# Kernel tuning notes

Measured on AMD Instinct MI355X. Metric: run time of the kernel, lower is better.

The kernel has to match this reference:

```python
import math
import jax, jax.numpy as jnp
import numpy as np

T = 4096
D_MODEL = 1024
NUM_HEADS = 16
HEAD_DIM = D_MODEL // NUM_HEADS


def setup_inputs() -> dict:
    key = jax.random.key(0)
    k_x, k_wqkv, k_wproj = jax.random.split(key, 3)
    # match eqx.nn.Linear init scale: U(-1/sqrt(in), 1/sqrt(in)); randn*small works too,
    # but keep magnitudes reasonable so softmax isn't saturated.
    s_in = 1.0 / math.sqrt(D_MODEL)
    x = jax.random.normal(k_x, (T, D_MODEL), dtype=jnp.float32)
    W_qkv = jax.random.normal(k_wqkv, (3 * D_MODEL, D_MODEL), dtype=jnp.float32) * s_in
    b_qkv = jnp.zeros((3 * D_MODEL,), dtype=jnp.float32)
    W_proj = jax.random.normal(k_wproj, (D_MODEL, D_MODEL), dtype=jnp.float32) * s_in
    b_proj = jnp.zeros((D_MODEL,), dtype=jnp.float32)
    return {"x": x, "W_qkv": W_qkv, "b_qkv": b_qkv, "W_proj": W_proj, "b_proj": b_proj}


def reference(x, W_qkv, b_qkv, W_proj, b_proj):
    T_, C = x.shape  # (seq, d_model)
    H, hd = NUM_HEADS, HEAD_DIM
    # c_attn: eqx Linear computes W @ x + b per token -> x @ W.T + b
    qkv = x @ W_qkv.T + b_qkv  # (T, 3C)
    q, k, v = jnp.split(qkv, 3, axis=1)
    # (T, C) -> (H, T, hd)
    q = q.reshape(T_, H, hd).swapaxes(0, 1)
    k = k.reshape(T_, H, hd).swapaxes(0, 1)
    v = v.reshape(T_, H, hd).swapaxes(0, 1)
    scores = jnp.einsum("htd,hsd->hts", q, k) / math.sqrt(hd)  # (H, T, T)
    causal = jnp.tril(jnp.ones((T_, T_), dtype=bool))
    scores = jnp.where(causal, scores, -jnp.inf)
    attn = jax.nn.softmax(scores, axis=-1)
    y = jnp.einsum("hts,hsd->htd", attn, v)  # (H, T, hd)
    y = y.swapaxes(0, 1).reshape(T_, C)
    y = y @ W_proj.T + b_proj
    return y
```

## Files before the change

kernel.cpp:

```cpp
#include <hip/hip_runtime.h>
#include <math.h>
#include <string.h>

#define T_SEQ 4096
#define DM 1024
#define NH 16
#define HD 64

typedef short s8v __attribute__((ext_vector_type(8)));
typedef float f4v __attribute__((ext_vector_type(4)));

__device__ inline unsigned short f2bf(float f) {
    unsigned u; memcpy(&u, &f, 4);
    u = u + 0x7fffu + ((u >> 16) & 1u);
    return (unsigned short)(u >> 16);
}

__device__ inline float bf2f(unsigned short s) {
    unsigned u = (unsigned)s << 16;
    float f; memcpy(&f, &u, 4);
    return f;
}

__device__ inline float exp2fn(float x) {
#if __has_builtin(__builtin_amdgcn_exp2f)
    return __builtin_amdgcn_exp2f(x);
#else
    return exp2f(x);
#endif
}

__device__ inline void gld_lds16(const void* g, void* l) {
    __builtin_amdgcn_global_load_lds(
        (const __attribute__((address_space(1))) void*)g,
        (__attribute__((address_space(3))) void*)l, 16, 0, 0);
}

__global__ __launch_bounds__(256)
void cvt3(const float* __restrict__ i0, unsigned short* __restrict__ o0, int n0,
          const float* __restrict__ i1, unsigned short* __restrict__ o1, int n1,
          const float* __restrict__ i2, unsigned short* __restrict__ o2, int n2) {
    int i = blockIdx.x * 256 + threadIdx.x;
    const float* in; unsigned short* out; int j;
    if (i < n0)           { in = i0; out = o0; j = i; }
    else if (i < n0 + n1) { in = i1; out = o1; j = i - n0; }
    else if (i < n0 + n1 + n2) { in = i2; out = o2; j = i - n0 - n1; }
    else return;
    const float4* p = (const float4*)(in + (size_t)j * 8);
    float4 a = p[0], b = p[1];
    unsigned short o[8] = {f2bf(a.x), f2bf(a.y), f2bf(a.z), f2bf(a.w),
                           f2bf(b.x), f2bf(b.y), f2bf(b.z), f2bf(b.w)};
    uint4 pk; memcpy(&pk, o, 16);
    *(uint4*)(out + (size_t)j * 8) = pk;
}

template<int MODE, int TN>
__global__ __launch_bounds__(256)
void gemm_bt_mfma(const unsigned short* __restrict__ A, const unsigned short* __restrict__ B,
                  const float* __restrict__ bias, void* __restrict__ Cout,
                  unsigned short* __restrict__ qbuf, unsigned short* __restrict__ kbuf2,
                  unsigned short* __restrict__ vT,
                  int M, int N, int K, int nbx, int patchw, int patchh) {
    constexpr int NF = TN / 32;
    __shared__ __align__(16) short As[2][4096];
    __shared__ __align__(16) short Bs[2][TN * 32];
    const int tid = threadIdx.x;
    const int w = tid >> 6, lane = tid & 63;
    const int wr = w >> 1, wc = w & 1;

    const int bl = blockIdx.x;
    const int xcd = bl & 7, ii = bl >> 3;
    const int pxn = nbx / patchw;
    const int bx = (xcd % pxn) * patchw + ii % patchw;
    const int by = (xcd / pxn) * patchh + ii / patchw;
    const int m0 = by * 128, n0 = bx * TN;

    const bool doA = (w < 2);
    const bool doStage = doA || ((w & 1) * 64 < TN);
    const unsigned short* src = doA ? A : B;
    const int rbase = (doA ? m0 : n0) + (w & 1) * 64;
    const unsigned short* gsrc = src + (size_t)(rbase + (lane & 15)) * K + ((lane >> 4) * 8);
    const int ldoff = ((w & 1) * 4) * 512;

    f4v acc[4][NF];
    #pragma unroll
    for (int i = 0; i < 4; ++i)
        #pragma unroll
        for (int j = 0; j < NF; ++j) acc[i][j] = (f4v){0.f, 0.f, 0.f, 0.f};

    auto stage = [&](short* base, int k0) {
        short* ldst = base + ldoff;
        #pragma unroll
        for (int i = 0; i < 4; ++i)
            gld_lds16(gsrc + (size_t)(i * 16) * K + k0, ldst + i * 512);
    };
    auto compute = [&](const short* Ab, const short* Bb) {
        s8v af[4], bfr[NF];
        #pragma unroll
        for (int i = 0; i < 4; ++i) af[i] = *(const s8v*)&Ab[((wr * 4 + i) * 64 + lane) * 8];
        #pragma unroll
        for (int j = 0; j < NF; ++j) bfr[j] = *(const s8v*)&Bb[((wc * NF + j) * 64 + lane) * 8];
        #pragma unroll
        for (int i = 0; i < 4; ++i)
            #pragma unroll
            for (int j = 0; j < NF; ++j)
                acc[i][j] = __builtin_amdgcn_mfma_f32_16x16x32_bf16(af[i], bfr[j], acc[i][j], 0, 0, 0);
    };

    if (doStage) stage(doA ? As[0] : Bs[0], 0);
    __syncthreads();
    for (int k0 = 0; k0 < K; k0 += 64) {
        if (doStage) stage(doA ? As[1] : Bs[1], k0 + 32);
        compute(As[0], Bs[0]);
        __syncthreads();
        if (doStage && (k0 + 64 < K)) stage(doA ? As[0] : Bs[0], k0 + 64);
        compute(As[1], Bs[1]);
        __syncthreads();
    }

    const int l15 = lane & 15, quad = lane >> 4;
    float bj[NF];
    #pragma unroll
    for (int j = 0; j < NF; ++j) bj[j] = bias[n0 + wc * (TN / 2) + j * 16 + l15];

    if (MODE == 2 && n0 >= 2 * DM) {
        const int tile = (m0 + wr * 64) >> 6;
        const int hh = ((n0 - 2 * DM) >> 6) + wc;
        #pragma unroll
        for (int i = 0; i < 4; ++i) {
            #pragma unroll
            for (int j = 0; j < NF; ++j) {
                unsigned short o[4];
                #pragma unroll
                for (int rg = 0; rg < 4; ++rg) o[rg] = f2bf(acc[i][j][rg] + bj[j]);
                unsigned long long pk; memcpy(&pk, o, 8);
                size_t off = (size_t)hh * 262144 + (size_t)tile * 4096
                           + (size_t)((j * 2 + (i >> 1)) * 64 + lane) * 8 + (i & 1) * 4;
                *(unsigned long long*)&vT[off] = pk;
            }
        }
    } else if (MODE == 2) {
        unsigned short* dst = (n0 < DM) ? qbuf : kbuf2;
        const int nb = (n0 < DM) ? n0 : n0 - DM;
        #pragma unroll
        for (int i = 0; i < 4; ++i) {
            #pragma unroll
            for (int rg = 0; rg < 4; ++rg) {
                int row = m0 + wr * 64 + i * 16 + quad * 4 + rg;
                #pragma unroll
                for (int j = 0; j < NF; ++j) {
                    int col = nb + wc * (TN / 2) + j * 16 + l15;
                    dst[(size_t)row * DM + col] = f2bf(acc[i][j][rg] + bj[j]);
                }
            }
        }
    } else {
        #pragma unroll
        for (int i = 0; i < 4; ++i) {
            #pragma unroll
            for (int rg = 0; rg < 4; ++rg) {
                int row = m0 + wr * 64 + i * 16 + quad * 4 + rg;
                #pragma unroll
                for (int j = 0; j < NF; ++j) {
                    int col = n0 + wc * (TN / 2) + j * 16 + l15;
                    ((float*)Cout)[(size_t)row * N + col] = acc[i][j][rg] + bj[j];
                }
            }
        }
    }
}

__device__ __forceinline__ void soft_step(f4v* st, bool diag, int qloc, int quad,
                                          float& lr, s8v& pf0, s8v& pf1) {
    const float C2  = 0.1803368851f;
    const float MC2 = 12.0f * 0.1803368851f;
    float sv[4][4];
    #pragma unroll
    for (int kb = 0; kb < 4; ++kb)
        #pragma unroll
        for (int rg = 0; rg < 4; ++rg) {
            float s = st[kb][rg];
            if (diag && (kb * 16 + quad * 4 + rg > qloc)) s = -3.0e38f;
            float t = exp2fn(fmaf(s, C2, -MC2));
            sv[kb][rg] = t;
            lr += t;
        }
    int pk[4][2];
    #pragma unroll
    for (int kb = 0; kb < 4; ++kb) {
        unsigned u0 = __float_as_uint(sv[kb][0]) + 0x8000u;
        unsigned u1 = __float_as_uint(sv[kb][1]) + 0x8000u;
        unsigned u2 = __float_as_uint(sv[kb][2]) + 0x8000u;
        unsigned u3 = __float_as_uint(sv[kb][3]) + 0x8000u;
        pk[kb][0] = (int)__builtin_amdgcn_perm(u1, u0, 0x07060302);
        pk[kb][1] = (int)__builtin_amdgcn_perm(u3, u2, 0x07060302);
    }
    int4 a = {pk[0][0], pk[0][1], pk[1][0], pk[1][1]};
    int4 b = {pk[2][0], pk[2][1], pk[3][0], pk[3][1]};
    memcpy(&pf0, &a, 16);
    memcpy(&pf1, &b, 16);
}

__global__ __launch_bounds__(256, 3)
void attn_mfma7(const unsigned short* __restrict__ qb,
                const unsigned short* __restrict__ kbf,
                const unsigned short* __restrict__ vT,
                unsigned short* __restrict__ y0,
                unsigned short* __restrict__ y1,
                unsigned short* __restrict__ y2,
                float* __restrict__ lsum) {
    const int b = blockIdx.x;
    const int par = b % 3;
    const int idx = b / 3;
    const int h = idx & 15, a = idx >> 4;
    const int tid = threadIdx.x;
    const int w = tid >> 6, lane = tid & 63;
    const int quad = lane >> 4, l15 = lane & 15;
    const int cq = h * HD;
    unsigned short* ypar = (par == 0) ? y0 : (par == 1) ? y1 : y2;
    float* lpar = lsum + ((size_t)par * NH + h) * T_SEQ;
    const unsigned short* vbase = vT + (size_t)h * 262144;

    __shared__ short KB[2][4096];
    __shared__ short VTs[2][4096];
    __shared__ short QB[8192];

    for (int ph = 0; ph < 2; ++ph) {
        const int qt = ph ? (31 - a) : a;
        const int q0 = qt * 128;
        const int kmax = 2 * qt + 1;
        const int nk = (kmax >= par) ? (kmax - par) / 3 + 1 : 0;
        const int kt0 = par * 64;

        __syncthreads();
        #pragma unroll
        for (int rr = 0; rr < 4; ++rr) {
            int ch = rr * 256 + tid;
            int qg = ch >> 7, hf = (ch >> 6) & 1, ln = ch & 63;
            gld_lds16(qb + (size_t)(q0 + qg * 16 + (ln & 15)) * DM + cq + hf * 32 + ((ln >> 4) << 3),
                      &QB[(ch & ~63) * 8]);
        }
        if (nk > 0) {
            #pragma unroll
            for (int rr = 0; rr < 2; ++rr) {
                int ch = rr * 256 + tid;
                int blk = ch >> 7, hf = (ch >> 6) & 1, ln = ch & 63;
                gld_lds16(kbf + (size_t)(kt0 + blk * 16 + (ln & 15)) * DM + cq + hf * 32 + ((ln >> 4) << 3),
                          &KB[0][(ch & ~63) * 8]);
                gld_lds16(vbase + (size_t)(kt0 >> 6) * 4096 + (size_t)ch * 8,
                          &VTs[0][(ch & ~63) * 8]);
            }
        }
        __syncthreads();

        s8v qf[2][2];
        #pragma unroll
        for (int g = 0; g < 2; ++g)
            #pragma unroll
            for (int hf = 0; hf < 2; ++hf)
                qf[g][hf] = *(const s8v*)&QB[((((g * 4 + w) * 2 + hf) * 64) + lane) * 8];

        f4v O0[4], O1[4];
        #pragma unroll
        for (int ob = 0; ob < 4; ++ob) {
            O0[ob] = (f4v){0.f, 0.f, 0.f, 0.f};
            O1[ob] = (f4v){0.f, 0.f, 0.f, 0.f};
        }
        float lr0 = 0.f, lr1 = 0.f;

        for (int i = 0; i < nk; ++i) {
            const int kt = par + 3 * i;
            const int p = i & 1;
            const bool g0a = (kt <= 2 * qt);
            const bool m0 = (kt == 2 * qt);
            const bool m1 = (kt == 2 * qt + 1);
            if (i < nk - 1) {
                const int k1 = kt0 + (i + 1) * 192;
                #pragma unroll
                for (int rr = 0; rr < 2; ++rr) {
                    int ch = rr * 256 + tid;
                    int blk = ch >> 7, hf = (ch >> 6) & 1, ln = ch & 63;
                    gld_lds16(kbf + (size_t)(k1 + blk * 16 + (ln & 15)) * DM + cq
                                  + hf * 32 + ((ln >> 4) << 3),
                              &KB[p ^ 1][(ch & ~63) * 8]);
                    gld_lds16(vbase + (size_t)(k1 >> 6) * 4096 + (size_t)ch * 8,
                              &VTs[p ^ 1][(ch & ~63) * 8]);
                }
            }

            f4v st0[4], st1[4];
            #pragma unroll
            for (int kb = 0; kb < 4; ++kb) {
                s8v k0f = *(const s8v*)&KB[p][((kb * 2 + 0) * 64 + lane) * 8];
                s8v k1f = *(const s8v*)&KB[p][((kb * 2 + 1) * 64 + lane) * 8];
                f4v c1 = (f4v){0.f, 0.f, 0.f, 0.f};
                c1 = __builtin_amdgcn_mfma_f32_16x16x32_bf16(k0f, qf[1][0], c1, 0, 0, 0);
                c1 = __builtin_amdgcn_mfma_f32_16x16x32_bf16(k1f, qf[1][1], c1, 0, 0, 0);
                st1[kb] = c1;
                if (g0a) {
                    f4v c0 = (f4v){0.f, 0.f, 0.f, 0.f};
                    c0 = __builtin_amdgcn_mfma_f32_16x16x32_bf16(k0f, qf[0][0], c0, 0, 0, 0);
                    c0 = __builtin_amdgcn_mfma_f32_16x16x32_bf16(k1f, qf[0][1], c0, 0, 0, 0);
                    st0[kb] = c0;
                }
            }

            s8v pf10, pf11, pf00, pf01;
            soft_step(st1, m1, w * 16 + l15, quad, lr1, pf10, pf11);
            if (g0a) soft_step(st0, m0, w * 16 + l15, quad, lr0, pf00, pf01);

            #pragma unroll
            for (int ob = 0; ob < 4; ++ob) {
                s8v v0f = *(const s8v*)&VTs[p][((ob * 2 + 0) * 64 + lane) * 8];
                s8v v1f = *(const s8v*)&VTs[p][((ob * 2 + 1) * 64 + lane) * 8];
                O1[ob] = __builtin_amdgcn_mfma_f32_16x16x32_bf16(v0f, pf10, O1[ob], 0, 0, 0);
                O1[ob] = __builtin_amdgcn_mfma_f32_16x16x32_bf16(v1f, pf11, O1[ob], 0, 0, 0);
                if (g0a) {
                    O0[ob] = __builtin_amdgcn_mfma_f32_16x16x32_bf16(v0f, pf00, O0[ob], 0, 0, 0);
                    O0[ob] = __builtin_amdgcn_mfma_f32_16x16x32_bf16(v1f, pf01, O0[ob], 0, 0, 0);
                }
            }
            __syncthreads();
        }

        lr0 += __shfl_xor(lr0, 16); lr0 += __shfl_xor(lr0, 32);
        lr1 += __shfl_xor(lr1, 16); lr1 += __shfl_xor(lr1, 32);
        #pragma unroll
        for (int g = 0; g < 2; ++g) {
            const f4v* O = g ? O1 : O0;
            int qrow = q0 + g * 64 + w * 16 + l15;
            size_t ybase = (size_t)qrow * DM + cq;
            #pragma unroll
            for (int ob = 0; ob < 4; ++ob) {
                unsigned short o[4];
                #pragma unroll
                for (int rg = 0; rg < 4; ++rg) o[rg] = f2bf(O[ob][rg]);
                unsigned long long pk; memcpy(&pk, o, 8);
                *(unsigned long long*)&ypar[ybase + ob * 16 + quad * 4] = pk;
            }
            if (quad == 0) lpar[qrow] = g ? lr1 : lr0;
        }
    }
}

__global__ __launch_bounds__(256)
void attn_combine3(const unsigned short* __restrict__ y0,
                   const unsigned short* __restrict__ y1,
                   const unsigned short* __restrict__ y2,
                   const float* __restrict__ lsum,
                   unsigned short* __restrict__ yout) {
    int i = blockIdx.x * 256 + threadIdx.x;
    int t = i >> 7, d8 = i & 127;
    int h = d8 >> 3;
    float l = lsum[(size_t)h * T_SEQ + t]
            + lsum[((size_t)NH + h) * T_SEQ + t]
            + lsum[((size_t)2 * NH + h) * T_SEQ + t];
    float inv = 1.f / l;
    size_t off = (size_t)t * DM + d8 * 8;
    uint4 ua = *(const uint4*)(y0 + off);
    uint4 ub = *(const uint4*)(y1 + off);
    uint4 uc = *(const uint4*)(y2 + off);
    const unsigned short* pa = (const unsigned short*)&ua;
    const unsigned short* pb = (const unsigned short*)&ub;
    const unsigned short* pc = (const unsigned short*)&uc;
    unsigned short o[8];
    #pragma unroll
    for (int k = 0; k < 8; ++k)
        o[k] = f2bf((bf2f(pa[k]) + bf2f(pb[k]) + bf2f(pc[k])) * inv);
    uint4 pk; memcpy(&pk, o, 16);
    *(uint4*)(yout + off) = pk;
}

extern "C" void kernel_launch(void* const* d_in, const int* in_sizes, int n_in,
                              void* d_out, int out_size, void* d_ws, size_t ws_size,
                              hipStream_t stream) {
    const float* x     = (const float*)d_in[0];
    const float* Wqkv  = (const float*)d_in[1];
    const float* bqkv  = (const float*)d_in[2];
    const float* Wproj = (const float*)d_in[3];
    const float* bproj = (const float*)d_in[4];
    float* out = (float*)d_out;

    char* ws = (char*)d_ws;
    unsigned short* qbuf  = (unsigned short*)(ws);
    unsigned short* kbuf  = (unsigned short*)(ws + ( 8u << 20));
    unsigned short* vTb   = (unsigned short*)(ws + (16u << 20));
    unsigned short* yattb = (unsigned short*)(ws + (24u << 20));
    unsigned short* wprjb = (unsigned short*)(ws + (32u << 20));
    float*          lsum  = (float*)         (ws + (34u << 20));
    unsigned short* xb    = (unsigned short*)(ws + (35u << 20));
    unsigned short* wqkvb = (unsigned short*)(ws + (43u << 20));
    unsigned short* y0p   = (unsigned short*)(ws + (35u << 20));
    unsigned short* y1p   = (unsigned short*)(ws + (43u << 20));
    unsigned short* y2p   = (unsigned short*)(ws + (51u << 20));

    dim3 blk(256);
    {
        int n0 = T_SEQ * DM / 8, n1 = 3 * DM * DM / 8, n2 = DM * DM / 8;
        cvt3<<<dim3((n0 + n1 + n2 + 255) / 256), blk, 0, stream>>>(
            x, xb, n0, Wqkv, wqkvb, n1, Wproj, wprjb, n2);
    }
    gemm_bt_mfma<2, 128><<<dim3(768), blk, 0, stream>>>(
        xb, wqkvb, bqkv, nullptr, qbuf, kbuf, vTb, T_SEQ, 3 * DM, DM, 24, 6, 16);
    attn_mfma7<<<dim3(768), blk, 0, stream>>>(qbuf, kbuf, vTb, y0p, y1p, y2p, lsum);
    attn_combine3<<<dim3(T_SEQ * DM / 8 / 256), blk, 0, stream>>>(y0p, y1p, y2p, lsum, yattb);
    gemm_bt_mfma<0, 64><<<dim3(512), blk, 0, stream>>>(
        yattb, wprjb, bproj, out, nullptr, nullptr, nullptr, T_SEQ, DM, DM, 16, 8, 8);
}
```

Measured before the change: 215.7 us.

## Generalize GEMM kernel to configurable tile and warp grid, enlarge tiles

Replaces the fixed 128xTN, 4-wave GEMM with a template over tile sizes and wave layout. The QKV projection now uses 256x192 tiles with 8 waves (256 blocks), and the output projection uses 128x128 tiles (256 blocks). Staging is spread across all waves, and the QKV epilogue routing to q/k/vT is now decided per column fragment. Larger tiles raise data reuse and cut global traffic, but they lower the block count to 256 per GEMM, which may leave CUs underused and increase register pressure.

```diff
diff --git a/kernel.cpp b/kernel.cpp
--- a/kernel.cpp
+++ b/kernel.cpp
@@ -54,115 +54,122 @@
     *(uint4*)(out + (size_t)j * 8) = pk;
 }
 
-template<int MODE, int TN>
-__global__ __launch_bounds__(256)
-void gemm_bt_mfma(const unsigned short* __restrict__ A, const unsigned short* __restrict__ B,
-                  const float* __restrict__ bias, void* __restrict__ Cout,
-                  unsigned short* __restrict__ qbuf, unsigned short* __restrict__ kbuf2,
-                  unsigned short* __restrict__ vT,
-                  int M, int N, int K, int nbx, int patchw, int patchh) {
-    constexpr int NF = TN / 32;
-    __shared__ __align__(16) short As[2][4096];
+template<int MODE, int TM, int TN, int WR, int WC>
+__global__ __launch_bounds__(WR * WC * 64, 1)
+void gemm_tile(const unsigned short* __restrict__ A, const unsigned short* __restrict__ B,
+               const float* __restrict__ bias, void* __restrict__ Cout,
+               unsigned short* __restrict__ qbuf, unsigned short* __restrict__ kbuf2,
+               unsigned short* __restrict__ vT,
+               int M, int N, int K, int nbx, int patchw, int patchh) {
+    constexpr int W  = WR * WC;
+    constexpr int MF = TM / WR / 16;
+    constexpr int NF = TN / WC / 16;
+    constexpr int NGA = TM / 16, NGB = TN / 16, NG = NGA + NGB;
+    __shared__ __align__(16) short As[2][TM * 32];
     __shared__ __align__(16) short Bs[2][TN * 32];
     const int tid = threadIdx.x;
     const int w = tid >> 6, lane = tid & 63;
-    const int wr = w >> 1, wc = w & 1;
+    const int wr = w / WC, wc = w % WC;
+    const int l15 = lane & 15, quad = lane >> 4;
 
     const int bl = blockIdx.x;
     const int xcd = bl & 7, ii = bl >> 3;
     const int pxn = nbx / patchw;
     const int bx = (xcd % pxn) * patchw + ii % patchw;
     const int by = (xcd / pxn) * patchh + ii / patchw;
-    const int m0 = by * 128, n0 = bx * TN;
-
-    const bool doA = (w < 2);
-    const bool doStage = doA || ((w & 1) * 64 < TN);
-    const unsigned short* src = doA ? A : B;
-    const int rbase = (doA ? m0 : n0) + (w & 1) * 64;
-    const unsigned short* gsrc = src + (size_t)(rbase + (lane & 15)) * K + ((lane >> 4) * 8);
-    const int ldoff = ((w & 1) * 4) * 512;
-
-    f4v acc[4][NF];
+    const int m0 = by * TM, n0 = bx * TN;
+
+    f4v acc[MF][NF];
     #pragma unroll
-    for (int i = 0; i < 4; ++i)
+    for (int i = 0; i < MF; ++i)
         #pragma unroll
         for (int j = 0; j < NF; ++j) acc[i][j] = (f4v){0.f, 0.f, 0.f, 0.f};
 
-    auto stage = [&](short* base, int k0) {
-        short* ldst = base + ldoff;
-        #pragma unroll
-        for (int i = 0; i < 4; ++i)
-            gld_lds16(gsrc + (size_t)(i * 16) * K + k0, ldst + i * 512);
+    auto stage = [&](int buf, int k0) {
+        for (int g = w; g < NG; g += W) {
+            const unsigned short* src;
+            short* dst;
+            if (g < NGA) {
+                src = A + (size_t)(m0 + g * 16 + l15) * K + quad * 8 + k0;
+                dst = &As[buf][g * 512];
+            } else {
+                src = B + (size_t)(n0 + (g - NGA) * 16 + l15) * K + quad * 8 + k0;
+                dst = &Bs[buf][(g - NGA) * 512];
+            }
+            gld_lds16(src, dst);
+        }
     };
-    auto compute = [&](const short* Ab, const short* Bb) {
-        s8v af[4], bfr[NF];
-        #pragma unroll
-        for (int i = 0; i < 4; ++i) af[i] = *(const s8v*)&Ab[((wr * 4 + i) * 64 + lane) * 8];
-        #pragma unroll
-        for (int j = 0; j < NF; ++j) bfr[j] = *(const s8v*)&Bb[((wc * NF + j) * 64 + lane) * 8];
-        #pragma unroll
-        for (int i = 0; i < 4; ++i)
+    auto compute = [&](int buf) {
+        s8v af[MF], bfr[NF];
+        #pragma unroll
+        for (int i = 0; i < MF; ++i)
+            af[i] = *(const s8v*)&As[buf][((wr * MF + i) * 64 + lane) * 8];
+        #pragma unroll
+        for (int j = 0; j < NF; ++j)
+            bfr[j] = *(const s8v*)&Bs[buf][((wc * NF + j) * 64 + lane) * 8];
+        #pragma unroll
+        for (int i = 0; i < MF; ++i)
             #pragma unroll
             for (int j = 0; j < NF; ++j)
                 acc[i][j] = __builtin_amdgcn_mfma_f32_16x16x32_bf16(af[i], bfr[j], acc[i][j], 0, 0, 0);
     };
 
-    if (doStage) stage(doA ? As[0] : Bs[0], 0);
+    stage(0, 0);
     __syncthreads();
     for (int k0 = 0; k0 < K; k0 += 64) {
-        if (doStage) stage(doA ? As[1] : Bs[1], k0 + 32);
-        compute(As[0], Bs[0]);
+        stage(1, k0 + 32);
+        compute(0);
         __syncthreads();
-        if (doStage && (k0 + 64 < K)) stage(doA ? As[0] : Bs[0], k0 + 64);
-        compute(As[1], Bs[1]);
+        if (k0 + 64 < K) stage(0, k0 + 64);
+        compute(1);
         __syncthreads();
     }
 
-    const int l15 = lane & 15, quad = lane >> 4;
     float bj[NF];
     #pragma unroll
-    for (int j = 0; j < NF; ++j) bj[j] = bias[n0 + wc * (TN / 2) + j * 16 + l15];
-
-    if (MODE == 2 && n0 >= 2 * DM) {
-        const int tile = (m0 + wr * 64) >> 6;
-        const int hh = ((n0 - 2 * DM) >> 6) + wc;
-        #pragma unroll
-        for (int i = 0; i < 4; ++i) {
-            #pragma unroll
-            for (int j = 0; j < NF; ++j) {
-                unsigned short o[4];
+    for (int j = 0; j < NF; ++j) bj[j] = bias[n0 + wc * (TN / WC) + j * 16 + l15];
+
+    if (MODE == 2) {
+        #pragma unroll
+        for (int j = 0; j < NF; ++j) {
+            const int ccol = n0 + wc * (TN / WC) + j * 16;
+            if (ccol >= 2 * DM) {
+                const int hh = (ccol - 2 * DM) >> 6;
+                const int ob = (ccol & 63) >> 4;
                 #pragma unroll
-                for (int rg = 0; rg < 4; ++rg) o[rg] = f2bf(acc[i][j][rg] + bj[j]);
-                unsigned long long pk; memcpy(&pk, o, 8);
-                size_t off = (size_t)hh * 262144 + (size_t)tile * 4096
-                           + (size_t)((j * 2 + (i >> 1)) * 64 + lane) * 8 + (i & 1) * 4;
-                *(unsigned long long*)&vT[off] = pk;
-            }
-        }
-    } else if (MODE == 2) {
-        unsigned short* dst = (n0 < DM) ? qbuf : kbuf2;
-        const int nb = (n0 < DM) ? n0 : n0 - DM;
-        #pragma unroll
-        for (int i = 0; i < 4; ++i) {
+                for (int i = 0; i < MF; ++i) {
+                    const int tile = (m0 + wr * (TM / WR)) / 64 + (i >> 2);
+                    const int it = i & 3;
+                    unsigned short o[4];
+                    #pragma unroll
+                    for (int rg = 0; rg < 4; ++rg) o[rg] = f2bf(acc[i][j][rg] + bj[j]);
+                    unsigned long long pk; memcpy(&pk, o, 8);
+                    size_t off = (size_t)hh * 262144 + (size_t)tile * 4096
+                               + (size_t)((ob * 2 + (it >> 1)) * 64 + lane) * 8 + (it & 1) * 4;
+                    *(unsigned long long*)&vT[off] = pk;
+                }
+            } else {
+                unsigned short* dst = (ccol < DM) ? qbuf : kbuf2;
+                const int col = (ccol < DM) ? (ccol + l15) : (ccol - DM + l15);
+                #pragma unroll
+                for (int i = 0; i < MF; ++i) {
+                    #pragma unroll
+                    for (int rg = 0; rg < 4; ++rg) {
+                        int row = m0 + wr * (TM / WR) + i * 16 + quad * 4 + rg;
+                        dst[(size_t)row * DM + col] = f2bf(acc[i][j][rg] + bj[j]);
+                    }
+                }
+            }
+        }
+    } else {
+        #pragma unroll
+        for (int i = 0; i < MF; ++i) {
             #pragma unroll
             for (int rg = 0; rg < 4; ++rg) {
-                int row = m0 + wr * 64 + i * 16 + quad * 4 + rg;
+                int row = m0 + wr * (TM / WR) + i * 16 + quad * 4 + rg;
                 #pragma unroll
                 for (int j = 0; j < NF; ++j) {
-                    int col = nb + wc * (TN / 2) + j * 16 + l15;
-                    dst[(size_t)row * DM + col] = f2bf(acc[i][j][rg] + bj[j]);
-                }
-            }
-        }
-    } else {
-        #pragma unroll
-        for (int i = 0; i < 4; ++i) {
-            #pragma unroll
-            for (int rg = 0; rg < 4; ++rg) {
-                int row = m0 + wr * 64 + i * 16 + quad * 4 + rg;
-                #pragma unroll
-                for (int j = 0; j < NF; ++j) {
-                    int col = n0 + wc * (TN / 2) + j * 16 + l15;
+                    int col = n0 + wc * (TN / WC) + j * 16 + l15;
                     ((float*)Cout)[(size_t)row * N + col] = acc[i][j][rg] + bj[j];
                 }
             }
@@ -394,16 +401,15 @@
     unsigned short* y1p   = (unsigned short*)(ws + (43u << 20));
     unsigned short* y2p   = (unsigned short*)(ws + (51u << 20));
 
-    dim3 blk(256);
     {
         int n0 = T_SEQ * DM / 8, n1 = 3 * DM * DM / 8, n2 = DM * DM / 8;
-        cvt3<<<dim3((n0 + n1 + n2 + 255) / 256), blk, 0, stream>>>(
+        cvt3<<<dim3((n0 + n1 + n2 + 255) / 256), dim3(256), 0, stream>>>(
             x, xb, n0, Wqkv, wqkvb, n1, Wproj, wprjb, n2);
     }
-    gemm_bt_mfma<2, 128><<<dim3(768), blk, 0, stream>>>(
-        xb, wqkvb, bqkv, nullptr, qbuf, kbuf, vTb, T_SEQ, 3 * DM, DM, 24, 6, 16);
-    attn_mfma7<<<dim3(768), blk, 0, stream>>>(qbuf, kbuf, vTb, y0p, y1p, y2p, lsum);
-    attn_combine3<<<dim3(T_SEQ * DM / 8 / 256), blk, 0, stream>>>(y0p, y1p, y2p, lsum, yattb);
-    gemm_bt_mfma<0, 64><<<dim3(512), blk, 0, stream>>>(
-        yattb, wprjb, bproj, out, nullptr, nullptr, nullptr, T_SEQ, DM, DM, 16, 8, 8);
-}
+    gemm_tile<2, 256, 192, 2, 4><<<dim3(256), dim3(512), 0, stream>>>(
+        xb, wqkvb, bqkv, nullptr, qbuf, kbuf, vTb, T_SEQ, 3 * DM, DM, 16, 8, 4);
+    attn_mfma7<<<dim3(768), dim3(256), 0, stream>>>(qbuf, kbuf, vTb, y0p, y1p, y2p, lsum);
+    attn_combine3<<<dim3(T_SEQ * DM / 8 / 256), dim3(256), 0, stream>>>(y0p, y1p, y2p, lsum, yattb);
+    gemm_tile<0, 128, 128, 2, 2><<<dim3(256), dim3(256), 0, stream>>>(
+        yattb, wprjb, bproj, out, nullptr, nullptr, nullptr, T_SEQ, DM, DM, 8, 4, 8);
+}
```

Result: no change. 214.5 us (-0.6%).
